# Performance work log

Measured on AMD Instinct MI355X. Metric: run time of the kernel, lower is better.

The kernel has to match this reference:

```python
import jax, jax.numpy as jnp
import numpy as np

ALPHA = 0.2          # LeakyReLU negative slope
THRESHOLD = 0.5      # adjacency threshold
NEG_INF = -9e15      # same fill value as torch source


def setup_inputs() -> dict:
    key = jax.random.key(0)
    k_in, k_adj, k_W, k_a = jax.random.split(key, 4)
    B, N, C = 32, 1024, 64
    inp = jax.random.normal(k_in, (B, N, C), dtype=jnp.float32)
    adj = jax.random.uniform(k_adj, (N, N), dtype=jnp.float32)
    # xavier_uniform with gain=1.414 (as in torch init)
    gain = 1.414
    lim_W = gain * np.sqrt(6.0 / (C + C))
    W = jax.random.uniform(k_W, (C, C), dtype=jnp.float32, minval=-lim_W, maxval=lim_W)
    lim_a = gain * np.sqrt(6.0 / (2 * C + 1))
    a = jax.random.uniform(k_a, (2 * C, 1), dtype=jnp.float32, minval=-lim_a, maxval=lim_a)
    return {"input": inp, "adj": adj, "W": W, "a": a}


def reference(input, adj, W, a):
    # h: [B, N, C]
    h = jnp.matmul(input, W)
    C = W.shape[0]
    a_src = a[:C, 0]   # applied to h_i (row / query node)
    a_dst = a[C:, 0]   # applied to h_j (col / neighbor node)
    # Algebraic decomposition of a^T [h_i || h_j]: outer-sum of two [B,N] vectors.
    s_src = jnp.matmul(h, a_src)  # [B, N]
    s_dst = jnp.matmul(h, a_dst)  # [B, N]
    e = jax.nn.leaky_relu(s_src[:, :, None] + s_dst[:, None, :], negative_slope=ALPHA)  # [B,N,N]
    mask = adj > THRESHOLD  # [N, N], broadcast over batch
    attention = jax.nn.softmax(jnp.where(mask[None, :, :], e, NEG_INF), axis=2)
    h_prime = jnp.matmul(attention, h)  # [B, N, C]
    return jax.nn.elu(h_prime)
```

## Files before the change

### kernel.cpp

```cpp
#include <hip/hip_runtime.h>
#include <math.h>

#define ALPHA 0.2f
#define LOG2E 1.4426950408889634f

constexpr int B = 32, N = 1024, C = 64;

typedef __attribute__((ext_vector_type(8))) short short8;
typedef __attribute__((ext_vector_type(16))) float floatx16;

static __device__ __forceinline__ unsigned bfu(float f) {
    return (__float_as_uint(f) + 0x8000u) >> 16;
}
static __device__ __forceinline__ unsigned pk2(float lo, float hi) {
    return ((__float_as_uint(hi) + 0x8000u) & 0xFFFF0000u) |
           ((__float_as_uint(lo) + 0x8000u) >> 16);
}

__global__ __launch_bounds__(256) void gat_pre(
    const float* __restrict__ input, const float* __restrict__ adj,
    const float* __restrict__ Wm, const float* __restrict__ a,
    unsigned short* __restrict__ hT, float* __restrict__ ssrc,
    float* __restrict__ sdst, unsigned long long* __restrict__ mask64)
{
    const int tid = threadIdx.x, lane = tid & 63, wave = tid >> 6;

    if (blockIdx.x < 1024) {
        const int mb = blockIdx.x;
#pragma unroll
        for (int t = 0; t < 4; ++t) {
            const int id = mb * 16 + wave * 4 + t;
            const int i = id >> 4, jc = id & 15;
            const float av = adj[(size_t)i * N + jc * 64 + lane];
            const unsigned long long bal = __ballot(av > 0.5f);
            if (lane == 0) mask64[i * 16 + jc] = bal;
        }
        return;
    }

    if (blockIdx.x < 2048) {
        __shared__ float wa_l[128];
        const int r0 = (blockIdx.x - 1024) * 32;

        if (tid < 128) {
            const int k = tid & 63, half = tid >> 6;
            const float* __restrict__ ar = a + half * 64;
            const float* __restrict__ wr = Wm + k * 64;
            float acc = 0.f;
#pragma unroll
            for (int c4 = 0; c4 < 16; ++c4) {
                const float4 wv = *(const float4*)&wr[c4 * 4];
                const float4 av = *(const float4*)&ar[c4 * 4];
                acc = fmaf(wv.x, av.x, fmaf(wv.y, av.y, fmaf(wv.z, av.z, fmaf(wv.w, av.w, acc))));
            }
            wa_l[half * 64 + k] = acc;
        }
        __syncthreads();

        const int row = r0 + (tid >> 3), seg = tid & 7;
        const float4 x0 = *(const float4*)&input[(size_t)row * 64 + seg * 8];
        const float4 x1 = *(const float4*)&input[(size_t)row * 64 + seg * 8 + 4];
        float vs = 0.f, vd = 0.f;
        const float4 w0 = *(const float4*)&wa_l[seg * 8];
        const float4 w1 = *(const float4*)&wa_l[seg * 8 + 4];
        const float4 d0 = *(const float4*)&wa_l[64 + seg * 8];
        const float4 d1 = *(const float4*)&wa_l[64 + seg * 8 + 4];
        vs = fmaf(x0.x, w0.x, fmaf(x0.y, w0.y, fmaf(x0.z, w0.z, fmaf(x0.w, w0.w, vs))));
        vs = fmaf(x1.x, w1.x, fmaf(x1.y, w1.y, fmaf(x1.z, w1.z, fmaf(x1.w, w1.w, vs))));
        vd = fmaf(x0.x, d0.x, fmaf(x0.y, d0.y, fmaf(x0.z, d0.z, fmaf(x0.w, d0.w, vd))));
        vd = fmaf(x1.x, d1.x, fmaf(x1.y, d1.y, fmaf(x1.z, d1.z, fmaf(x1.w, d1.w, vd))));
        vs += __shfl_xor(vs, 1, 64); vd += __shfl_xor(vd, 1, 64);
        vs += __shfl_xor(vs, 2, 64); vd += __shfl_xor(vd, 2, 64);
        vs += __shfl_xor(vs, 4, 64); vd += __shfl_xor(vd, 4, 64);
        if (seg == 0) { ssrc[row] = vs * LOG2E; sdst[row] = vd * LOG2E; }
        return;
    }

    {
        const int hb = blockIdx.x - 2048;
        const int b  = hb >> 2;
        const int j0 = (hb & 3) * 256;
        const int wc = wave & 1, ws = wave >> 1;
        const int n32 = lane & 31, kh = lane >> 5;

        short8 wfr[4];
#pragma unroll
        for (int q = 0; q < 4; ++q)
#pragma unroll
            for (int e = 0; e < 8; ++e)
                wfr[q][e] = (short)bfu(Wm[(q * 16 + kh * 8 + e) * 64 + wc * 32 + n32]);

        const float* __restrict__ inb = input + (size_t)b * 1024 * 64;

#pragma unroll
        for (int tt = 0; tt < 4; ++tt) {
            const int jb = j0 + ws * 128 + tt * 32;
            floatx16 acc = {};
#pragma unroll
            for (int q = 0; q < 4; ++q) {
                const float4 x0 = *(const float4*)&inb[(size_t)(jb + n32) * 64 + q * 16 + kh * 8];
                const float4 x1 = *(const float4*)&inb[(size_t)(jb + n32) * 64 + q * 16 + kh * 8 + 4];
                union { uint4 u; short8 s; } bf;
                bf.u.x = pk2(x0.x, x0.y); bf.u.y = pk2(x0.z, x0.w);
                bf.u.z = pk2(x1.x, x1.y); bf.u.w = pk2(x1.z, x1.w);
                acc = __builtin_amdgcn_mfma_f32_32x32x16_bf16(wfr[q], bf.s, acc, 0, 0, 0);
            }
#pragma unroll
            for (int r = 0; r < 16; ++r) {
                const int rc = (r & 3) + 8 * (r >> 2) + 4 * kh;
                hT[((size_t)(b * 64 + wc * 32 + rc)) * 1024 + jb + n32] = (unsigned short)bfu(acc[r]);
            }
        }
    }
}

__global__ __launch_bounds__(256, 4) void gat_attn(
    const unsigned short* __restrict__ hTg, const float* __restrict__ ssrc,
    const float* __restrict__ sdst, const unsigned long long* __restrict__ mask64,
    float* __restrict__ out)
{
    __shared__ __align__(16) float accb[2][16 * 64];
    __shared__ float psum_s[4 * 32];

    const int tid = threadIdx.x, lane = tid & 63, wave = tid >> 6;
    const int b  = blockIdx.x & 31;
    const int i0 = (blockIdx.x >> 5) * 32;
    const int wc = wave & 1;
    const int wj = wave >> 1;
    const int c0 = wc * 32;
    const int n32 = lane & 31, kh = lane >> 5;

    const float ssq = ssrc[b * N + i0 + n32];
    const float* __restrict__ sdb = sdst + b * N;
    const unsigned short* __restrict__ hTb = hTg + ((size_t)(b * 64 + c0 + n32)) * 1024;
    const unsigned long long* __restrict__ mrow = mask64 + (size_t)(i0 + n32) * 16;

    floatx16 acc = {};
    float psacc = 0.f;

    for (int t = 0; t < 8; ++t) {
        const int jt = wj * 8 + t;
        const int jb = jt * 64;

        short8 hfr[4];
        float4 sa[4], sb[4];
#pragma unroll
        for (int q = 0; q < 4; ++q) {
            hfr[q] = *(const short8*)&hTb[jb + q * 16 + kh * 8];
            sa[q]  = *(const float4*)&sdb[jb + q * 16 + kh * 8];
            sb[q]  = *(const float4*)&sdb[jb + q * 16 + kh * 8 + 4];
        }
        const uint2 mw = *(const uint2*)&mrow[jt];

#pragma unroll
        for (int q = 0; q < 4; ++q) {
            const unsigned mword = (q < 2) ? mw.x : mw.y;
            const unsigned msh = mword >> ((q & 1) * 16 + kh * 8);
            const float sv[8] = {sa[q].x, sa[q].y, sa[q].z, sa[q].w,
                                 sb[q].x, sb[q].y, sb[q].z, sb[q].w};
            float p[8];
#pragma unroll
            for (int e = 0; e < 8; ++e) {
                float tv = ssq + sv[e];
                tv = fmaxf(tv, ALPHA * tv);
                tv = ((msh >> e) & 1u) ? tv : -200.f;
                p[e] = exp2f(tv);
                psacc += p[e];
            }
            union { uint4 u; short8 s; } af;
            af.u.x = pk2(p[0], p[1]); af.u.y = pk2(p[2], p[3]);
            af.u.z = pk2(p[4], p[5]); af.u.w = pk2(p[6], p[7]);
            acc = __builtin_amdgcn_mfma_f32_32x32x16_bf16(af.s, hfr[q], acc, 0, 0, 0);
        }
    }

    psacc += __shfl_xor(psacc, 32, 64);
    if (lane < 32) psum_s[wave * 32 + lane] = psacc;
    if (wj == 1) {
#pragma unroll
        for (int r = 0; r < 16; ++r) accb[wc][r * 64 + lane] = acc[r];
    }
    __syncthreads();

    if (wj == 0) {
#pragma unroll
        for (int r = 0; r < 16; ++r) {
            const float sum = acc[r] + accb[wc][r * 64 + lane];
            const int row = (r & 3) + 8 * (r >> 2) + 4 * kh;
            const float ps = psum_s[row] + psum_s[64 + row];
            const float hp = sum / ps;
            const float o = hp > 0.f ? hp : __expf(hp) - 1.f;
            out[((size_t)(b * N + i0 + row)) * 64 + c0 + n32] = o;
        }
    }
}

extern "C" void kernel_launch(void* const* d_in, const int* in_sizes, int n_in,
                              void* d_out, int out_size, void* d_ws, size_t ws_size,
                              hipStream_t stream) {
    const float* input = (const float*)d_in[0];
    const float* adj   = (const float*)d_in[1];
    const float* Wm    = (const float*)d_in[2];
    const float* a     = (const float*)d_in[3];
    float* out = (float*)d_out;

    char* ws = (char*)d_ws;
    unsigned short* hT = (unsigned short*)ws;
    float* ssrc = (float*)(ws + 4194304);
    float* sdst = (float*)(ws + 4194304 + 131072);
    unsigned long long* mask64 = (unsigned long long*)(ws + 4194304 + 2 * 131072);

    gat_pre<<<2176, 256, 0, stream>>>(input, adj, Wm, a, hT, ssrc, sdst, mask64);
    gat_attn<<<1024, 256, 0, stream>>>(hT, ssrc, sdst, mask64, out);
}
```

Measured before the change: 110.4 us.

## Split j range across all four waves in attention, widen h projection grid

```diff
diff --git a/kernel.cpp b/kernel.cpp
--- a/kernel.cpp
+++ b/kernel.cpp
@@ -78,9 +78,10 @@
 
     {
         const int hb = blockIdx.x - 2048;
-        const int b  = hb >> 2;
-        const int j0 = (hb & 3) * 256;
-        const int wc = wave & 1, ws = wave >> 1;
+        const int b  = hb >> 4;
+        const int jseg = (hb & 15) * 64;
+        const int wc = wave & 1, jsub = wave >> 1;
+        const int jb = jseg + jsub * 32;
         const int n32 = lane & 31, kh = lane >> 5;
 
         short8 wfr[4];
@@ -91,25 +92,20 @@
                 wfr[q][e] = (short)bfu(Wm[(q * 16 + kh * 8 + e) * 64 + wc * 32 + n32]);
 
         const float* __restrict__ inb = input + (size_t)b * 1024 * 64;
-
-#pragma unroll
-        for (int tt = 0; tt < 4; ++tt) {
-            const int jb = j0 + ws * 128 + tt * 32;
-            floatx16 acc = {};
-#pragma unroll
-            for (int q = 0; q < 4; ++q) {
-                const float4 x0 = *(const float4*)&inb[(size_t)(jb + n32) * 64 + q * 16 + kh * 8];
-                const float4 x1 = *(const float4*)&inb[(size_t)(jb + n32) * 64 + q * 16 + kh * 8 + 4];
-                union { uint4 u; short8 s; } bf;
-                bf.u.x = pk2(x0.x, x0.y); bf.u.y = pk2(x0.z, x0.w);
-                bf.u.z = pk2(x1.x, x1.y); bf.u.w = pk2(x1.z, x1.w);
-                acc = __builtin_amdgcn_mfma_f32_32x32x16_bf16(wfr[q], bf.s, acc, 0, 0, 0);
-            }
-#pragma unroll
-            for (int r = 0; r < 16; ++r) {
-                const int rc = (r & 3) + 8 * (r >> 2) + 4 * kh;
-                hT[((size_t)(b * 64 + wc * 32 + rc)) * 1024 + jb + n32] = (unsigned short)bfu(acc[r]);
-            }
+        floatx16 acc = {};
+#pragma unroll
+        for (int q = 0; q < 4; ++q) {
+            const float4 x0 = *(const float4*)&inb[(size_t)(jb + n32) * 64 + q * 16 + kh * 8];
+            const float4 x1 = *(const float4*)&inb[(size_t)(jb + n32) * 64 + q * 16 + kh * 8 + 4];
+            union { uint4 u; short8 s; } bf;
+            bf.u.x = pk2(x0.x, x0.y); bf.u.y = pk2(x0.z, x0.w);
+            bf.u.z = pk2(x1.x, x1.y); bf.u.w = pk2(x1.z, x1.w);
+            acc = __builtin_amdgcn_mfma_f32_32x32x16_bf16(wfr[q], bf.s, acc, 0, 0, 0);
+        }
+#pragma unroll
+        for (int r = 0; r < 16; ++r) {
+            const int rc = (r & 3) + 8 * (r >> 2) + 4 * kh;
+            hT[((size_t)(b * 64 + wc * 32 + rc)) * 1024 + jb + n32] = (unsigned short)bfu(acc[r]);
         }
     }
 }
@@ -119,34 +115,34 @@
     const float* __restrict__ sdst, const unsigned long long* __restrict__ mask64,
     float* __restrict__ out)
 {
-    __shared__ __align__(16) float accb[2][16 * 64];
-    __shared__ float psum_s[4 * 32];
+    __shared__ __align__(16) float acc_l[4][32 * 68];
+    __shared__ float psum_l[4][32];
 
     const int tid = threadIdx.x, lane = tid & 63, wave = tid >> 6;
     const int b  = blockIdx.x & 31;
     const int i0 = (blockIdx.x >> 5) * 32;
-    const int wc = wave & 1;
-    const int wj = wave >> 1;
-    const int c0 = wc * 32;
+    const int wj = wave;
     const int n32 = lane & 31, kh = lane >> 5;
 
     const float ssq = ssrc[b * N + i0 + n32];
     const float* __restrict__ sdb = sdst + b * N;
-    const unsigned short* __restrict__ hTb = hTg + ((size_t)(b * 64 + c0 + n32)) * 1024;
+    const unsigned short* __restrict__ hT0 = hTg + ((size_t)(b * 64 + n32)) * 1024;
+    const unsigned short* __restrict__ hT1 = hT0 + 32 * 1024;
     const unsigned long long* __restrict__ mrow = mask64 + (size_t)(i0 + n32) * 16;
 
-    floatx16 acc = {};
+    floatx16 acc0 = {}, acc1 = {};
     float psacc = 0.f;
 
-    for (int t = 0; t < 8; ++t) {
-        const int jt = wj * 8 + t;
+    for (int t = 0; t < 4; ++t) {
+        const int jt = wj * 4 + t;
         const int jb = jt * 64;
 
-        short8 hfr[4];
+        short8 bf0[4], bf1[4];
         float4 sa[4], sb[4];
 #pragma unroll
         for (int q = 0; q < 4; ++q) {
-            hfr[q] = *(const short8*)&hTb[jb + q * 16 + kh * 8];
+            bf0[q] = *(const short8*)&hT0[jb + q * 16 + kh * 8];
+            bf1[q] = *(const short8*)&hT1[jb + q * 16 + kh * 8];
             sa[q]  = *(const float4*)&sdb[jb + q * 16 + kh * 8];
             sb[q]  = *(const float4*)&sdb[jb + q * 16 + kh * 8 + 4];
         }
@@ -170,28 +166,48 @@
             union { uint4 u; short8 s; } af;
             af.u.x = pk2(p[0], p[1]); af.u.y = pk2(p[2], p[3]);
             af.u.z = pk2(p[4], p[5]); af.u.w = pk2(p[6], p[7]);
-            acc = __builtin_amdgcn_mfma_f32_32x32x16_bf16(af.s, hfr[q], acc, 0, 0, 0);
+            acc0 = __builtin_amdgcn_mfma_f32_32x32x16_bf16(af.s, bf0[q], acc0, 0, 0, 0);
+            acc1 = __builtin_amdgcn_mfma_f32_32x32x16_bf16(af.s, bf1[q], acc1, 0, 0, 0);
         }
     }
 
     psacc += __shfl_xor(psacc, 32, 64);
-    if (lane < 32) psum_s[wave * 32 + lane] = psacc;
-    if (wj == 1) {
-#pragma unroll
-        for (int r = 0; r < 16; ++r) accb[wc][r * 64 + lane] = acc[r];
+    if (lane < 32) psum_l[wave][lane] = psacc;
+
+#pragma unroll
+    for (int r = 0; r < 16; ++r) {
+        const int row = (r & 3) + 8 * (r >> 2) + 4 * kh;
+        acc_l[wave][row * 68 + n32]      = acc0[r];
+        acc_l[wave][row * 68 + 32 + n32] = acc1[r];
     }
     __syncthreads();
 
-    if (wj == 0) {
-#pragma unroll
-        for (int r = 0; r < 16; ++r) {
-            const float sum = acc[r] + accb[wc][r * 64 + lane];
-            const int row = (r & 3) + 8 * (r >> 2) + 4 * kh;
-            const float ps = psum_s[row] + psum_s[64 + row];
-            const float hp = sum / ps;
-            const float o = hp > 0.f ? hp : __expf(hp) - 1.f;
-            out[((size_t)(b * N + i0 + row)) * 64 + c0 + n32] = o;
-        }
+    {
+        const int i = tid >> 3, c8 = (tid & 7) * 8;
+        float4 u0 = {0.f,0.f,0.f,0.f}, u1 = {0.f,0.f,0.f,0.f};
+#pragma unroll
+        for (int w = 0; w < 4; ++w) {
+            const float4 v0 = *(const float4*)&acc_l[w][i * 68 + c8];
+            const float4 v1 = *(const float4*)&acc_l[w][i * 68 + c8 + 4];
+            u0.x += v0.x; u0.y += v0.y; u0.z += v0.z; u0.w += v0.w;
+            u1.x += v1.x; u1.y += v1.y; u1.z += v1.z; u1.w += v1.w;
+        }
+        const float ps = psum_l[0][i] + psum_l[1][i] + psum_l[2][i] + psum_l[3][i];
+        const float inv = 1.f / ps;
+        float o[8] = {u0.x * inv, u0.y * inv, u0.z * inv, u0.w * inv,
+                      u1.x * inv, u1.y * inv, u1.z * inv, u1.w * inv};
+        float4 w0, w1;
+        w0.x = o[0] > 0.f ? o[0] : __expf(o[0]) - 1.f;
+        w0.y = o[1] > 0.f ? o[1] : __expf(o[1]) - 1.f;
+        w0.z = o[2] > 0.f ? o[2] : __expf(o[2]) - 1.f;
+        w0.w = o[3] > 0.f ? o[3] : __expf(o[3]) - 1.f;
+        w1.x = o[4] > 0.f ? o[4] : __expf(o[4]) - 1.f;
+        w1.y = o[5] > 0.f ? o[5] : __expf(o[5]) - 1.f;
+        w1.z = o[6] > 0.f ? o[6] : __expf(o[6]) - 1.f;
+        w1.w = o[7] > 0.f ? o[7] : __expf(o[7]) - 1.f;
+        float* dst = out + ((size_t)(b * N + i0 + i)) * 64 + c8;
+        *(float4*)dst = w0;
+        *(float4*)(dst + 4) = w1;
     }
 }
 
@@ -210,6 +226,6 @@
     float* sdst = (float*)(ws + 4194304 + 131072);
     unsigned long long* mask64 = (unsigned long long*)(ws + 4194304 + 2 * 131072);
 
-    gat_pre<<<2176, 256, 0, stream>>>(input, adj, Wm, a, hT, ssrc, sdst, mask64);
+    gat_pre<<<2560, 256, 0, stream>>>(input, adj, Wm, a, hT, ssrc, sdst, mask64);
     gat_attn<<<1024, 256, 0, stream>>>(hT, ssrc, sdst, mask64, out);
 }
```

Result: slower. 118.5 us (+7.4%).
